# Kernel tuning notes

Measured on AMD Instinct MI355X. Metric: run time of the kernel, lower is better.

The kernel has to match this reference:

```python
import jax, jax.numpy as jnp
import numpy as np

N_E = 4096
E_DIM = 256
BETA = 0.25


def setup_inputs() -> dict:
    key = jax.random.key(0)
    k1, k2 = jax.random.split(key)
    z = jax.random.normal(k1, (2, E_DIM, 8, 32, 32), dtype=jnp.float32)
    # torch: embedding.weight.data.uniform_(-1/n_e, 1/n_e)
    embedding_weight = jax.random.uniform(
        k2, (N_E, E_DIM), dtype=jnp.float32, minval=-1.0 / N_E, maxval=1.0 / N_E)
    ema_embedding = jnp.zeros((N_E, E_DIM), dtype=jnp.float32)
    return {"z": z, "embedding_weight": embedding_weight, "ema_embedding": ema_embedding}


def reference(z, embedding_weight, ema_embedding):
    sg = jax.lax.stop_gradient
    # [B, C, D, H, W] -> [B, D, H, W, C]
    zp = jnp.transpose(z, (0, 2, 3, 4, 1))
    zf = zp.reshape(-1, E_DIM)  # [N, e_dim]
    # pairwise squared distances: ||z||^2 + ||e||^2 - 2 z e^T  -> [N, n_e]
    d = (jnp.sum(zf * zf, axis=1, keepdims=True)
         + jnp.sum(embedding_weight * embedding_weight, axis=1)
         - 2.0 * jnp.matmul(zf, embedding_weight.T))
    min_encoding_indices = jnp.argmin(d, axis=1)  # [N]
    min_encodings = jax.nn.one_hot(min_encoding_indices, N_E, dtype=zf.dtype)  # [N, n_e]
    # one_hot @ W == gather of codebook rows
    z_q = embedding_weight[min_encoding_indices].reshape(zp.shape)
    loss = (jnp.mean((sg(z_q) - zp) ** 2)
            + BETA * jnp.mean((z_q - sg(zp)) ** 2))
    # straight-through estimator
    z_q_st = zp + sg(z_q - zp)
    # EMA buffer update (torch does this under no_grad)
    ema_new = BETA * ema_embedding + (1.0 - BETA) * sg(embedding_weight)
    e_mean = jnp.mean(min_encodings, axis=0)
    perplexity = jnp.exp(-jnp.sum(e_mean * jnp.log(e_mean + 1e-10)))
    z_q_out = jnp.transpose(z_q_st, (0, 4, 1, 2, 3))
    z_out = jnp.transpose(zp, (0, 4, 1, 2, 3))
    return (loss, z_q_out, perplexity, min_encodings,
            min_encoding_indices[:, None], z_out, ema_new)
```

## Files before the change

kernel.cpp:

```cpp
#include <hip/hip_runtime.h>
#include <math.h>


#define N_E    4096
#define EDIM   256
#define SPAT   8192
#define NROWS  16384
#define ZELEMS 4194304
#define NCHUNK 32
#define NLOSSPARTS 16384

#define OFF_LOSS    0
#define OFF_ZQ      1
#define OFF_PERP    4194305
#define OFF_ONEHOT  4194306
#define OFF_IDX     71303170
#define OFF_ZOUT    71319554
#define OFF_EMA     75513858

#define SCR_WH_F   4
#define SCR_BI_F   71319556
#define SCR_BDD_F  71843844
#define SCR_ZH_F   72892420

#define MARG 1.3e-4f
#define GAPM 1.3e-4f

#define PB_W0   0
#define PB_Z0   1024
#define PB_N0   1536
#define PB_H0   1664
#define PB_TOT  1668

typedef unsigned short u16;
typedef short short8 __attribute__((ext_vector_type(8)));
typedef float f32x4 __attribute__((ext_vector_type(4)));
typedef const void __attribute__((address_space(1)))* gas1;
typedef void __attribute__((address_space(3)))* las3;
#define GLOAD16(g, l) __builtin_amdgcn_global_load_lds((gas1)(g), (las3)(l), 16, 0, 0)

__device__ __forceinline__ u16 f2bf(float f) {
    unsigned u = __float_as_uint(f);
    return (u16)((u + 0x7fffu + ((u >> 16) & 1u)) >> 16);
}
__device__ __forceinline__ float bf2f(u16 h) {
    return __uint_as_float(((unsigned)h) << 16);
}

__global__ __launch_bounds__(256) void prep_all_kernel(
        const float* __restrict__ W, const float* __restrict__ ema,
        const float* __restrict__ z,
        u16* __restrict__ wh,
        float* __restrict__ se, float* __restrict__ out_ema,
        u16* __restrict__ zh, float* __restrict__ sz,
        int* __restrict__ ghist) {
    __shared__ float t[128][65];
    __shared__ float szp[4][128];
    const int bx  = blockIdx.x;
    const int tid = threadIdx.x;

    if (bx < PB_Z0) {
        const size_t tt = (size_t)bx * 256 + tid;
        const int code = (int)(tt >> 6);
        const int lane = tid & 63;
        const float4 v = *(const float4*)(W + tt * 4);

        u16 h0 = f2bf(v.x), h1 = f2bf(v.y), h2 = f2bf(v.z), h3 = f2bf(v.w);
        uint2 hp;
        hp.x = (unsigned)h0 | ((unsigned)h1 << 16); hp.y = (unsigned)h2 | ((unsigned)h3 << 16);
        *(uint2*)(wh + tt * 4) = hp;

        const float4 e4 = *(const float4*)(ema + tt * 4);
        float4 o4;
        o4.x = 0.25f * e4.x + 0.75f * v.x;
        o4.y = 0.25f * e4.y + 0.75f * v.y;
        o4.z = 0.25f * e4.z + 0.75f * v.z;
        o4.w = 0.25f * e4.w + 0.75f * v.w;
        *(float4*)(out_ema + tt * 4) = o4;

        float s = v.x * v.x + v.y * v.y + v.z * v.z + v.w * v.w;
        #pragma unroll
        for (int off = 32; off > 0; off >>= 1) s += __shfl_down(s, off);
        if (lane == 0) se[code] = s;
    } else if (bx < PB_N0) {
        const int sub = bx - PB_Z0;
        const int sp0 = (sub & 127) * 64, c0 = ((sub >> 7) & 1) * 128, b = sub >> 8;
        const int wid = tid >> 6, lane = tid & 63;
        const float* zb = z + (size_t)b * (EDIM * SPAT);
        #pragma unroll
        for (int it = 0; it < 32; ++it) {
            const int cl = wid + 4 * it;
            t[cl][lane] = zb[(size_t)(c0 + cl) * SPAT + sp0 + lane];
        }
        __syncthreads();
        #pragma unroll
        for (int it = 0; it < 16; ++it) {
            const int r = wid + 4 * it;
            const float v0 = t[2 * lane][r], v1 = t[2 * lane + 1][r];
            const u16 h0 = f2bf(v0), h1 = f2bf(v1);
            const size_t row = (size_t)b * SPAT + sp0 + r;
            ((unsigned*)zh)[row * 128 + (c0 >> 1) + lane] = (unsigned)h0 | ((unsigned)h1 << 16);
        }
    } else if (bx < PB_H0) {
        const int r0 = (bx - PB_N0) * 128;
        const int bb = r0 >> 13;
        const int sp0 = r0 & (SPAT - 1);
        const float* zb = z + (size_t)bb * (EDIM * SPAT) + sp0;
        const int lr = tid & 127, kh = tid >> 7;
        #pragma unroll
        for (int h = 0; h < 2; ++h) {
            const int kq = kh * 2 + h;
            float s = 0.f;
            const float* p = zb + lr + (size_t)(kq * 64) * SPAT;
            for (int k = 0; k < 64; ++k) {
                float v = p[(size_t)k * SPAT];
                s += v * v;
            }
            szp[kq][lr] = s;
        }
        __syncthreads();
        if (tid < 128)
            sz[r0 + tid] = ((szp[0][tid] + szp[1][tid]) + szp[2][tid]) + szp[3][tid];
    } else {
        const int base = (bx - PB_H0) * 1024;
        #pragma unroll
        for (int j = 0; j < 4; ++j) ghist[base + j * 256 + tid] = 0;
    }
}

__global__ __launch_bounds__(256, 4) void argmin_kernel(
        const u16* __restrict__ zh, const u16* __restrict__ wh,
        const float* __restrict__ se, const float* __restrict__ sz,
        float* __restrict__ bDD, int* __restrict__ bI,
        float* __restrict__ out_onehot) {
    __shared__ u16 sW[2][128][32];
    __shared__ u16 sZ[2][128][32];
    __shared__ float mD[2][128];
    __shared__ int   mI[2][128];
    __shared__ float mD2[2][128];

    const int tid = threadIdx.x;
    const int wid = tid >> 6, lane = tid & 63;
    const int wm = wid >> 1, wn = wid & 1;
    const int lq = lane >> 4, lr = lane & 15;
    const int chunk = blockIdx.y;
    const int rbase = blockIdx.x * 128;
    const int cbase = chunk * 128;

    const u16* gw[2]; const u16* gz[2];
    #pragma unroll
    for (int j = 0; j < 2; ++j) {
        const int o = j * 256 + tid;
        const int row = o >> 2, g = o & 3, u = g ^ ((row >> 1) & 3);
        gw[j] = wh + (size_t)(cbase + row) * EDIM + u * 8;
        gz[j] = zh + (size_t)(rbase + row) * EDIM + u * 8;
    }

    char* sWb = (char*)&sW[0][0][0];
    char* sZb = (char*)&sZ[0][0][0];

    int aoff[4], boff[4];
    #pragma unroll
    for (int tt = 0; tt < 4; ++tt) {
        const int cl = wn * 64 + tt * 16 + lr;
        aoff[tt] = cl * 64 + (lq ^ ((cl >> 1) & 3)) * 16;
        const int rl = wm * 64 + tt * 16 + lr;
        boff[tt] = rl * 64 + (lq ^ ((rl >> 1) & 3)) * 16;
    }

    f32x4 acc[4][4];
    #pragma unroll
    for (int ci = 0; ci < 4; ++ci)
        #pragma unroll
        for (int rj = 0; rj < 4; ++rj) {
            f32x4 zzz = {0.f, 0.f, 0.f, 0.f};
            acc[ci][rj] = zzz;
        }

    #define STAGE(b) do {                                                      \
        _Pragma("unroll")                                                      \
        for (int j = 0; j < 2; ++j) {                                          \
            GLOAD16(gw[j], sWb + (b) * 8192 + (j * 256 + wid * 64) * 16);      \
            GLOAD16(gz[j], sZb + (b) * 8192 + (j * 256 + wid * 64) * 16);      \
            gw[j] += 32; gz[j] += 32;                                          \
        }                                                                      \
    } while (0)

    STAGE(0);
    __syncthreads();

    for (int k0 = 0; k0 < 8; ++k0) {
        const int cur = k0 & 1;
        if (k0 < 7) STAGE(cur ^ 1);

        const char* wbase = sWb + cur * 8192;
        const char* zbase = sZb + cur * 8192;
        short8 zb[4];
        #pragma unroll
        for (int rj = 0; rj < 4; ++rj)
            zb[rj] = *(const short8*)(zbase + boff[rj]);
        #pragma unroll
        for (int ci = 0; ci < 4; ++ci) {
            const short8 wah = *(const short8*)(wbase + aoff[ci]);
            #pragma unroll
            for (int rj = 0; rj < 4; ++rj)
                acc[ci][rj] = __builtin_amdgcn_mfma_f32_16x16x32_bf16(wah, zb[rj], acc[ci][rj], 0, 0, 0);
        }
        __syncthreads();
    }
    #undef STAGE

    f32x4 sev[4];
    #pragma unroll
    for (int ci = 0; ci < 4; ++ci)
        sev[ci] = *(const f32x4*)(se + cbase + wn * 64 + ci * 16 + lq * 4);

    #pragma unroll
    for (int rj = 0; rj < 4; ++rj) {
        const int rloc = wm * 64 + rj * 16 + lr;
        const float szr = sz[rbase + rloc];
        float b1 = 3.4e38f, b2 = 3.4e38f; int bi1 = 0x7fffffff;
        #pragma unroll
        for (int ci = 0; ci < 4; ++ci) {
            #pragma unroll
            for (int r = 0; r < 4; ++r) {
                const float q = (szr + sev[ci][r]) - 2.0f * acc[ci][rj][r];
                const int code = cbase + wn * 64 + ci * 16 + lq * 4 + r;
                if (q < b1 || (q == b1 && code < bi1)) {
                    b2 = b1; b1 = q; bi1 = code;
                } else if (q < b2) {
                    b2 = q;
                }
            }
        }
        #pragma unroll
        for (int mask = 16; mask <= 32; mask <<= 1) {
            const float od1 = __shfl_xor(b1, mask);
            const int   oi1 = __shfl_xor(bi1, mask);
            const float od2 = __shfl_xor(b2, mask);
            const bool ot = (od1 < b1) || (od1 == b1 && oi1 < bi1);
            if (ot) { b2 = fminf(b1, od2); b1 = od1; bi1 = oi1; }
            else    { b2 = fminf(b2, od1); }
        }
        if (lq == 0) {
            mD[wn][rloc]  = b1;
            mI[wn][rloc]  = bi1;
            mD2[wn][rloc] = b2;
        }
    }
    __syncthreads();
    if (tid < 128) {
        const float d0 = mD[0][tid], d1 = mD[1][tid];
        const int   i0 = mI[0][tid], i1 = mI[1][tid];
        const float s0 = mD2[0][tid], s1 = mD2[1][tid];
        float dm, sm; int im;
        if (d1 < d0 || (d1 == d0 && i1 < i0)) { dm = d1; im = i1; sm = fminf(s1, d0); }
        else                                  { dm = d0; im = i0; sm = fminf(s0, d1); }
        const int row = rbase + tid;
        float2 p; p.x = dm; p.y = sm;
        *(float2*)(bDD + (size_t)row * 64 + chunk * 2) = p;
        bI[(size_t)row * 32 + chunk] = im;
    }

    {
        const int slice = blockIdx.x * 32 + blockIdx.y;
        float* oh = out_onehot + (size_t)slice * 16384;
        const float4 z4 = {0.f, 0.f, 0.f, 0.f};
        #pragma unroll
        for (int it = 0; it < 16; ++it)
            *(float4*)(oh + it * 1024 + tid * 4) = z4;
    }
}

__global__ __launch_bounds__(128) void resolve_kernel(
        const float* __restrict__ z, const float* __restrict__ W,
        const float* __restrict__ se, const float* __restrict__ sz,
        const float* __restrict__ bDD, const int* __restrict__ bI,
        int* __restrict__ idx_ws, float* __restrict__ out_idx,
        float* __restrict__ out_onehot) {
    __shared__ float zr[EDIM];
    __shared__ float rd[128];
    __shared__ int   ri[128];
    __shared__ unsigned smask;
    __shared__ int swin, sskip;
    const int row = blockIdx.x;
    const int tid = threadIdx.x;

    if (tid < 64) {
        const int c = tid & 31;
        const float2 dd = *(const float2*)(bDD + (size_t)row * 64 + c * 2);
        const int    i1 = bI[(size_t)row * 32 + c];
        const float d1 = dd.x;
        float b1 = dd.x, b2 = dd.y; int j1 = i1;
        #pragma unroll
        for (int mask = 16; mask > 0; mask >>= 1) {
            const float od1 = __shfl_xor(b1, mask);
            const int   oj1 = __shfl_xor(j1, mask);
            const float od2 = __shfl_xor(b2, mask);
            const bool ot = (od1 < b1) || (od1 == b1 && oj1 < j1);
            if (ot) { b2 = fminf(b1, od2); b1 = od1; j1 = oj1; }
            else    { b2 = fminf(b2, od1); }
        }
        const unsigned long long m = __ballot(d1 <= b1 + MARG);
        if (tid == 0) {
            smask = (unsigned)(m & 0xffffffffu);
            swin  = j1;
            sskip = (b2 - b1 > GAPM) ? 1 : 0;
        }
    }
    __syncthreads();

    if (sskip) {
        if (tid == 0) {
            idx_ws[row]  = swin;
            out_idx[row] = (float)swin;
            out_onehot[(size_t)row * N_E + swin] = 1.0f;
        }
        return;
    }

    {
        const int b = row >> 13, sp = row & (SPAT - 1);
        zr[tid]       = z[(size_t)b * (EDIM * SPAT) + (size_t)tid * SPAT + sp];
        zr[tid + 128] = z[(size_t)b * (EDIM * SPAT) + (size_t)(tid + 128) * SPAT + sp];
    }
    __syncthreads();

    const float szr = sz[row];
    unsigned cmask = smask;
    float best = 3.4e38f; int bi = 0x7fffffff;
    while (cmask) {
        const int cc = __ffs(cmask) - 1;
        cmask &= cmask - 1;
        const int code = cc * 128 + tid;
        const float* wr = W + (size_t)code * EDIM;
        float s = 0.f;
        for (int k = 0; k < EDIM; ++k) s += zr[k] * wr[k];
        const float q = (szr + se[code]) - 2.0f * s;
        if (q < best || (q == best && code < bi)) { best = q; bi = code; }
    }
    rd[tid] = best; ri[tid] = bi;
    __syncthreads();
    for (int off = 64; off > 0; off >>= 1) {
        if (tid < off) {
            const float od = rd[tid + off]; const int oi = ri[tid + off];
            if (od < rd[tid] || (od == rd[tid] && oi < ri[tid])) {
                rd[tid] = od; ri[tid] = oi;
            }
        }
        __syncthreads();
    }
    if (tid == 0) {
        const int ii = ri[0];
        idx_ws[row]  = ii;
        out_idx[row] = (float)ii;
        out_onehot[(size_t)row * N_E + ii] = 1.0f;
    }
}

__global__ __launch_bounds__(1024) void hist_kernel(const int* __restrict__ idx,
                                                    int* __restrict__ ghist) {
    __shared__ int lh[N_E];
    const int tid = threadIdx.x;
    for (int i = tid; i < N_E; i += 1024) lh[i] = 0;
    __syncthreads();
    atomicAdd(&lh[idx[blockIdx.x * 1024 + tid]], 1);
    __syncthreads();
    for (int c = tid; c < N_E; c += 1024) {
        const int v = lh[c];
        if (v) atomicAdd(&ghist[c], v);
    }
}

__global__ __launch_bounds__(256) void outputs_kernel(
        const float* __restrict__ z, const float* __restrict__ W,
        const int* __restrict__ idx,
        float* __restrict__ zq_out, float* __restrict__ z_out,
        double* __restrict__ loss_parts) {
    const int t  = blockIdx.x * 256 + threadIdx.x;
    const float zv = z[t];
    const int sp = t & (SPAT - 1);
    const int c  = (t >> 13) & 255;
    const int b  = t >> 21;
    const int n  = (b << 13) + sp;
    const int id = idx[n];
    const float e    = W[id * EDIM + c];
    const float diff = e - zv;
    zq_out[t] = zv + diff;
    z_out[t]  = zv;

    double ds = (double)(diff * diff);
    #pragma unroll
    for (int off = 32; off > 0; off >>= 1) ds += __shfl_down(ds, off);
    __shared__ double bsum[4];
    const int lane = threadIdx.x & 63, w = threadIdx.x >> 6;
    if (lane == 0) bsum[w] = ds;
    __syncthreads();
    if (threadIdx.x == 0)
        loss_parts[blockIdx.x] = bsum[0] + bsum[1] + bsum[2] + bsum[3];
}

__global__ __launch_bounds__(1024) void final_kernel(
        const int* __restrict__ ghist, const double* __restrict__ loss_parts,
        float* __restrict__ out_loss, float* __restrict__ out_perp) {
    __shared__ float ps[1024];
    __shared__ double ls[1024];
    const int tid = threadIdx.x;

    float s = 0.f;
    for (int c = tid; c < N_E; c += 1024) {
        const float p = (float)ghist[c] * (1.0f / (float)NROWS);
        s += p * logf(p + 1e-10f);
    }
    double l = 0.0;
    for (int c = tid; c < NLOSSPARTS; c += 1024) l += loss_parts[c];
    ps[tid] = s;
    ls[tid] = l;
    __syncthreads();
    for (int off = 512; off > 0; off >>= 1) {
        if (tid < off) {
            ps[tid] += ps[tid + off];
            ls[tid] += ls[tid + off];
        }
        __syncthreads();
    }
    if (tid == 0) {
        *out_perp = expf(-ps[0]);
        const float m = (float)(ls[0] / (double)ZELEMS);
        *out_loss = m + 0.25f * m;
    }
}

extern "C" void kernel_launch(void* const* d_in, const int* in_sizes, int n_in,
                              void* d_out, int out_size, void* d_ws, size_t ws_size,
                              hipStream_t stream) {
    const float* z   = (const float*)d_in[0];
    const float* W   = (const float*)d_in[1];
    const float* ema = (const float*)d_in[2];
    float* out = (float*)d_out;

    float* out_loss   = out + OFF_LOSS;
    float* out_zq     = out + OFF_ZQ;
    float* out_perp   = out + OFF_PERP;
    float* out_onehot = out + OFF_ONEHOT;
    float* out_idx    = out + OFF_IDX;
    float* out_z      = out + OFF_ZOUT;
    float* out_ema    = out + OFF_EMA;

    u16*   wh  = (u16*)(out + SCR_WH_F);
    int*   bI  = (int*)(out + SCR_BI_F);
    float* bDD = out + SCR_BDD_F;
    u16*   zh  = (u16*)(out + SCR_ZH_F);

    char* ws = (char*)d_ws;
    float*  se    = (float*)ws;
    float*  sz    = (float*)(ws + 16384);
    int*    idxb  = (int*)  (ws + 81920);
    double* lossp = (double*)(ws + 147456);
    int*    ghist = (int*)  (ws + 278528);

    prep_all_kernel<<<PB_TOT, 256, 0, stream>>>(W, ema, z, wh, se, out_ema,
                                                zh, sz, ghist);
    argmin_kernel<<<dim3(NROWS / 128, NCHUNK), 256, 0, stream>>>(
        zh, wh, se, sz, bDD, bI, out_onehot);
    resolve_kernel<<<NROWS, 128, 0, stream>>>(z, W, se, sz, bDD, bI,
                                              idxb, out_idx, out_onehot);
    hist_kernel<<<16, 1024, 0, stream>>>(idxb, ghist);
    outputs_kernel<<<ZELEMS / 256, 256, 0, stream>>>(z, W, idxb, out_zq, out_z,
                                                     lossp);
    final_kernel<<<1, 1024, 0, stream>>>(ghist, lossp, out_loss, out_perp);
}
```

Before: 518.2 us.

## Refine argmin candidates per code and stage row-major fp32 z for resolve

The resolve step now checks each chunk's best and second-best bf16 distance against a global threshold. Chunks whose runner-up is also within the margin get a full 128-code fp32 rescan, while chunks where only the best is close contribute just that one code, checked by a single thread. Rows with exactly one candidate and no full chunks skip the fp32 work entirely. The prep kernel also writes a row-major fp32 copy of z into workspace, when it is large enough, so resolve can load a row contiguously instead of with strided gathers. This adds an extra 16 MB write in prep and relies on the workspace being big enough.

```diff
diff --git a/kernel.cpp b/kernel.cpp
--- a/kernel.cpp
+++ b/kernel.cpp
@@ -23,8 +23,10 @@
 #define SCR_BDD_F  71843844
 #define SCR_ZH_F   72892420
 
+#define ZT_OFF     294912
+#define ZT_BYTES   16777216
+
 #define MARG 1.3e-4f
-#define GAPM 1.3e-4f
 
 #define PB_W0   0
 #define PB_Z0   1024
@@ -53,7 +55,7 @@
         u16* __restrict__ wh,
         float* __restrict__ se, float* __restrict__ out_ema,
         u16* __restrict__ zh, float* __restrict__ sz,
-        int* __restrict__ ghist) {
+        int* __restrict__ ghist, float* __restrict__ zt) {
     __shared__ float t[128][65];
     __shared__ float szp[4][128];
     const int bx  = blockIdx.x;
@@ -100,6 +102,10 @@
             const u16 h0 = f2bf(v0), h1 = f2bf(v1);
             const size_t row = (size_t)b * SPAT + sp0 + r;
             ((unsigned*)zh)[row * 128 + (c0 >> 1) + lane] = (unsigned)h0 | ((unsigned)h1 << 16);
+            if (zt) {
+                float2 p; p.x = v0; p.y = v1;
+                *(float2*)(zt + row * 256 + c0 + 2 * lane) = p;
+            }
         }
     } else if (bx < PB_H0) {
         const int r0 = (bx - PB_N0) * 128;
@@ -276,50 +282,55 @@
         const float* __restrict__ z, const float* __restrict__ W,
         const float* __restrict__ se, const float* __restrict__ sz,
         const float* __restrict__ bDD, const int* __restrict__ bI,
+        const float* __restrict__ zt,
         int* __restrict__ idx_ws, float* __restrict__ out_idx,
         float* __restrict__ out_onehot) {
     __shared__ float zr[EDIM];
     __shared__ float rd[128];
     __shared__ int   ri[128];
-    __shared__ unsigned smask;
-    __shared__ int swin, sskip;
+    __shared__ int   scode[32];
+    __shared__ unsigned sfull;
+    __shared__ int   sncand;
     const int row = blockIdx.x;
     const int tid = threadIdx.x;
 
     if (tid < 64) {
         const int c = tid & 31;
         const float2 dd = *(const float2*)(bDD + (size_t)row * 64 + c * 2);
-        const int    i1 = bI[(size_t)row * 32 + c];
-        const float d1 = dd.x;
-        float b1 = dd.x, b2 = dd.y; int j1 = i1;
-        #pragma unroll
-        for (int mask = 16; mask > 0; mask >>= 1) {
-            const float od1 = __shfl_xor(b1, mask);
-            const int   oj1 = __shfl_xor(j1, mask);
-            const float od2 = __shfl_xor(b2, mask);
-            const bool ot = (od1 < b1) || (od1 == b1 && oj1 < j1);
-            if (ot) { b2 = fminf(b1, od2); b1 = od1; j1 = oj1; }
-            else    { b2 = fminf(b2, od1); }
-        }
-        const unsigned long long m = __ballot(d1 <= b1 + MARG);
+        float g1 = dd.x;
+        #pragma unroll
+        for (int mask = 16; mask > 0; mask >>= 1)
+            g1 = fminf(g1, __shfl_xor(g1, mask));
+        const float thr = g1 + MARG;
+        const unsigned long long mful = __ballot(dd.y <= thr);
+        const unsigned long long mcnd = __ballot(dd.x <= thr && dd.y > thr);
+        const unsigned fm = (unsigned)(mful & 0xffffffffu);
+        const unsigned cm = (unsigned)(mcnd & 0xffffffffu);
+        if (tid < 32 && ((cm >> tid) & 1u)) {
+            const int pos = __popc(cm & ((1u << tid) - 1u));
+            scode[pos] = bI[(size_t)row * 32 + tid];
+        }
+        if (tid == 0) { sfull = fm; sncand = __popc(cm); }
+    }
+    __syncthreads();
+
+    const unsigned fmask = sfull;
+    const int ncand = sncand;
+
+    if (fmask == 0u && ncand == 1) {
         if (tid == 0) {
-            smask = (unsigned)(m & 0xffffffffu);
-            swin  = j1;
-            sskip = (b2 - b1 > GAPM) ? 1 : 0;
-        }
-    }
-    __syncthreads();
-
-    if (sskip) {
-        if (tid == 0) {
-            idx_ws[row]  = swin;
-            out_idx[row] = (float)swin;
-            out_onehot[(size_t)row * N_E + swin] = 1.0f;
+            const int ii = scode[0];
+            idx_ws[row]  = ii;
+            out_idx[row] = (float)ii;
+            out_onehot[(size_t)row * N_E + ii] = 1.0f;
         }
         return;
     }
 
-    {
+    if (zt) {
+        zr[tid]       = zt[(size_t)row * EDIM + tid];
+        zr[tid + 128] = zt[(size_t)row * EDIM + tid + 128];
+    } else {
         const int b = row >> 13, sp = row & (SPAT - 1);
         zr[tid]       = z[(size_t)b * (EDIM * SPAT) + (size_t)tid * SPAT + sp];
         zr[tid + 128] = z[(size_t)b * (EDIM * SPAT) + (size_t)(tid + 128) * SPAT + sp];
@@ -327,8 +338,17 @@
     __syncthreads();
 
     const float szr = sz[row];
-    unsigned cmask = smask;
     float best = 3.4e38f; int bi = 0x7fffffff;
+
+    if (tid < ncand) {
+        const int code = scode[tid];
+        const float* wr = W + (size_t)code * EDIM;
+        float s = 0.f;
+        for (int k = 0; k < EDIM; ++k) s += zr[k] * wr[k];
+        const float q = (szr + se[code]) - 2.0f * s;
+        if (q < best || (q == best && code < bi)) { best = q; bi = code; }
+    }
+    unsigned cmask = fmask;
     while (cmask) {
         const int cc = __ffs(cmask) - 1;
         cmask &= cmask - 1;
@@ -458,12 +478,14 @@
     int*    idxb  = (int*)  (ws + 81920);
     double* lossp = (double*)(ws + 147456);
     int*    ghist = (int*)  (ws + 278528);
+    float*  zt    = (ws_size >= (size_t)ZT_OFF + ZT_BYTES)
+                        ? (float*)(ws + ZT_OFF) : (float*)0;
 
     prep_all_kernel<<<PB_TOT, 256, 0, stream>>>(W, ema, z, wh, se, out_ema,
-                                                zh, sz, ghist);
+                                                zh, sz, ghist, zt);
     argmin_kernel<<<dim3(NROWS / 128, NCHUNK), 256, 0, stream>>>(
         zh, wh, se, sz, bDD, bI, out_onehot);
-    resolve_kernel<<<NROWS, 128, 0, stream>>>(z, W, se, sz, bDD, bI,
+    resolve_kernel<<<NROWS, 128, 0, stream>>>(z, W, se, sz, bDD, bI, zt,
                                               idxb, out_idx, out_onehot);
     hist_kernel<<<16, 1024, 0, stream>>>(idxb, ghist);
     outputs_kernel<<<ZELEMS / 256, 256, 0, stream>>>(z, W, idxb, out_zq, out_z,
```

Result: faster. 459.7 us (-11.3%).
